# Kernel optimization log

Hardware: AMD Instinct MI355X
Metric: run time of the kernel (lower is better)

## Reference

```python
import jax, jax.numpy as jnp
import numpy as np

K = 16
NUM_RBF = 32
MAX_DIST = 24.0
OUT_DIM = 256
_SPACING = MAX_DIST / (NUM_RBF - 1)
GAMMA = 1.0 / (_SPACING * _SPACING + 1e-08)
CENTERS = jnp.linspace(0.0, MAX_DIST, NUM_RBF)


def setup_inputs() -> dict:
    key = jax.random.key(0)
    k1, k2, k3 = jax.random.split(key, 3)
    B, M = 64, 1024
    # scale coords so pairwise distances span roughly [0, MAX_DIST]
    ligand_coords = jax.random.normal(k1, (B, M, 3), dtype=jnp.float32) * 8.0
    ligand_mask = jax.random.randint(k2, (B, M), 0, 2) > 0
    proj_w = jax.random.normal(k3, (OUT_DIM, K * NUM_RBF), dtype=jnp.float32) * 0.05
    return {"ligand_coords": ligand_coords, "ligand_mask": ligand_mask, "proj_w": proj_w}


def reference(ligand_coords, ligand_mask, proj_w):
    B, M, _ = ligand_coords.shape
    x = ligand_coords.astype(jnp.float32)
    # pairwise euclidean distances via the gram trick (avoids [B,M,M,3])
    sq = jnp.sum(x * x, axis=-1)                      # [B, M]
    gram = jnp.einsum('bid,bjd->bij', x, x)           # [B, M, M]
    d2 = sq[:, :, None] + sq[:, None, :] - 2.0 * gram
    dists = jnp.sqrt(jnp.maximum(d2, 1e-12))          # [B, M, M]
    eye = jnp.eye(M, dtype=bool)[None]
    valid_pair = ligand_mask[:, :, None] & ligand_mask[:, None, :]
    invalid = eye | ~valid_pair
    dists = jnp.where(invalid, jnp.inf, dists)
    # k smallest distances per atom
    neg_topk, _ = jax.lax.top_k(-dists, K)            # [B, M, K]
    topk = -neg_topk
    d_padded = jnp.where(jnp.isfinite(topk), topk, MAX_DIST)
    # RBF embed
    diff = d_padded[..., None] - CENTERS              # [B, M, K, NUM_RBF]
    rbf = jnp.exp(-GAMMA * diff * diff)
    rbf_flat = rbf.reshape(B, M, K * NUM_RBF)
    out = jnp.einsum('bmf,of->bmo', rbf_flat, proj_w)
    return out * ligand_mask[..., None].astype(out.dtype)
```

## Files before the change

kernel.cpp:

```cpp
#include <hip/hip_runtime.h>
#include <hip/hip_bf16.h>
#include <math.h>

#define MDIM 1024
#define QTOT 65536
#define KTOP 16
#define ODIM 256
#define FDIM 512

typedef float f32x4 __attribute__((ext_vector_type(4)));
typedef short s16x8 __attribute__((ext_vector_type(8)));
typedef unsigned u32x4 __attribute__((ext_vector_type(4)));

#define VMIN(a,b)  ({float r_; asm("v_min_f32 %0,%1,%2":"=v"(r_):"v"(a),"v"(b)); r_;})
#define VMAX(a,b)  ({float r_; asm("v_max_f32 %0,%1,%2":"=v"(r_):"v"(a),"v"(b)); r_;})
#define VEXP2(x)   ({float r_; asm("v_exp_f32 %0,%1":"=v"(r_):"v"(x)); r_;})

__device__ __forceinline__ int read_mask(const void* m, int i, bool is8) {
  return is8 ? (int)((const unsigned char*)m)[i] : ((const int*)m)[i];
}

__device__ __forceinline__ unsigned pack2(float lo, float hi) {
  __hip_bfloat162 h = __float22bfloat162_rn(make_float2(lo, hi));
  unsigned u;
  __builtin_memcpy(&u, &h, sizeof(u));
  return u;
}

#define CEx(A,i,j) { float mn_ = VMIN(A[i], A[j]); float mx_ = VMAX(A[i], A[j]); A[i] = mn_; A[j] = mx_; }
#define SORT8(A) \
  CEx(A,0,1) CEx(A,2,3) CEx(A,4,5) CEx(A,6,7) \
  CEx(A,0,2) CEx(A,1,3) CEx(A,4,6) CEx(A,5,7) \
  CEx(A,1,2) CEx(A,5,6) \
  CEx(A,0,4) CEx(A,1,5) CEx(A,2,6) CEx(A,3,7) \
  CEx(A,2,4) CEx(A,3,5) \
  CEx(A,1,2) CEx(A,3,4) CEx(A,5,6)
#define CLEAN16(A) \
  CEx(A,0,8) CEx(A,1,9) CEx(A,2,10) CEx(A,3,11) CEx(A,4,12) CEx(A,5,13) CEx(A,6,14) CEx(A,7,15) \
  CEx(A,0,4) CEx(A,1,5) CEx(A,2,6)  CEx(A,3,7)  CEx(A,8,12) CEx(A,9,13) CEx(A,10,14) CEx(A,11,15) \
  CEx(A,0,2) CEx(A,1,3) CEx(A,4,6)  CEx(A,5,7)  CEx(A,8,10) CEx(A,9,11) CEx(A,12,14) CEx(A,13,15) \
  CEx(A,0,1) CEx(A,2,3) CEx(A,4,5)  CEx(A,6,7)  CEx(A,8,9)  CEx(A,10,11) CEx(A,12,13) CEx(A,14,15)

__global__ __launch_bounds__(256) void wconv_kernel(
    const float* __restrict__ W, u32x4* __restrict__ Wb)
{
  int slot = blockIdx.x * 256 + threadIdx.x;
  int cg = slot >> 10;
  int rem = slot & 1023;
  int s = rem >> 6, l = rem & 63;
  int col = cg * 16 + (l & 15);
  int kk = s * 32 + (l >> 4) * 8;
  const float4* p = (const float4*)(W + (size_t)col * FDIM + kk);
  float4 a = p[0], b = p[1];
  u32x4 u0;
  u0[0] = pack2(a.x, a.y); u0[1] = pack2(a.z, a.w);
  u0[2] = pack2(b.x, b.y); u0[3] = pack2(b.z, b.w);
  Wb[(size_t)(cg * 16 + s) * 64 + l] = u0;
}

constexpr double SPd = 24.0 / 31.0;
constexpr double SP2d = SPd * SPd;
constexpr float ALPHA = (float)(-(SP2d / (SP2d + 1e-8)) * 1.4426950408889634);
constexpr float INV_SP = (float)(1.0 / SPd);

__device__ __forceinline__ void gen_cell(u32x4* Ab, int rf, int rowlo, int s, float d0) {
  float d = (d0 < 0.f) ? 1.0e9f : d0;
  float u = d * INV_SP;
  float C1 = (-2.0f * ALPHA) * u;
  float C0 = ALPHA * u * u;
  #pragma unroll
  for (int c8 = 0; c8 < 4; ++c8) {
    u32x4 ch;
    #pragma unroll
    for (int q = 0; q < 4; ++q) {
      const int j0 = c8 * 8 + q * 2;
      float e0 = VEXP2(fmaf(C1, (float)j0,       C0) + ALPHA * (float)(j0 * j0));
      float e1 = VEXP2(fmaf(C1, (float)(j0 + 1), C0) + ALPHA * (float)((j0 + 1) * (j0 + 1)));
      ch[q] = pack2(e0, e1);
    }
    Ab[rf * 1040 + s * 65 + c8 * 16 + rowlo] = ch;
  }
}

__global__ __launch_bounds__(512, 6) void fused_kernel(
    const float* __restrict__ coords, const void* __restrict__ mask,
    const u32x4* __restrict__ Wb, float* __restrict__ out)
{
  __shared__ __align__(16) char raw[66560];
  __shared__ float dvals[64][17];
  __shared__ int s_cnt;
  __shared__ int s_is8;

  float4* pts = (float4*)raw;
  short* posof = (short*)(raw + 16384);
  float* ST = (float*)(raw + 18432);
  u32x4* Ab = (u32x4*)raw;

  const int tid = threadIdx.x;
  const int lane = tid & 63;
  const int wv = tid >> 6;
  const int bid = blockIdx.x;
  const int batch = bid >> 4;
  const int qchunk = bid & 15;

  if (tid == 0) { s_cnt = 0; s_is8 = 0; }
  __syncthreads();
  {
    unsigned w = ((const unsigned*)mask)[tid & 255];
    if (w > 1u) atomicOr(&s_is8, 1);
  }
  __syncthreads();
  const bool is8 = (s_is8 != 0);

  const float* cb = coords + (size_t)batch * MDIM * 3;
  const int mbase = batch * MDIM;

  #pragma unroll
  for (int r = 0; r < 2; ++r) {
    int a = r * 512 + tid;
    int v = read_mask(mask, mbase + a, is8);
    float x = cb[a*3+0], y = cb[a*3+1], z = cb[a*3+2];
    float S = fmaf(z, z, fmaf(y, y, x * x));
    unsigned long long bal = __ballot(v != 0);
    int base = 0;
    if (lane == 0) base = atomicAdd(&s_cnt, __popcll(bal));
    base = __shfl(base, 0);
    int pos = base + __popcll(bal & ((1ull << lane) - 1ull));
    if (v) {
      float4 p; p.x = x; p.y = y; p.z = z; p.w = S;
      pts[pos] = p;
    }
    posof[a] = (short)(v ? pos : -1);
  }
  __syncthreads();
  const int cnt = s_cnt;
  const int cntP = (cnt + 63) & ~63;
  for (int i = cnt + tid; i < cntP; i += 512) {
    float4 p; p.x = 0.f; p.y = 0.f; p.z = 0.f; p.w = 3.0e38f;
    pts[i] = p;
  }
  __syncthreads();

  const int qlocal = qchunk * 64 + lane;
  const float qx = cb[qlocal*3+0], qy = cb[qlocal*3+1], qz = cb[qlocal*3+2];
  const float Q = fmaf(qz, qz, fmaf(qy, qy, qx * qx));
  const float m2x = -2.0f * qx, m2y = -2.0f * qy, m2z = -2.0f * qz;
  const int selfpos = posof[qlocal];
  const int G = cntP >> 3;
  const int sbase = wv * G;

  float t[16];
  #pragma unroll
  for (int i = 0; i < 16; ++i) t[i] = 3.0e38f;

  for (int b = 0; b < G; b += 8) {
    float s[8];
    #pragma unroll
    for (int i = 0; i < 8; ++i) {
      const int idx = sbase + b + i;
      float4 p = pts[idx];
      float d = fmaf(p.z, m2z, fmaf(p.y, m2y, fmaf(p.x, m2x, p.w)));
      s[i] = (idx == selfpos) ? 3.0e38f : d;
    }
    SORT8(s)
    #pragma unroll
    for (int i = 0; i < 8; ++i) t[8 + i] = VMIN(t[8 + i], s[7 - i]);
    CLEAN16(t)
  }

  {
    float* dst = ST + (wv * 64 + lane) * 17;
    #pragma unroll
    for (int i = 0; i < 16; ++i) dst[i] = t[i];
  }
  __syncthreads();

  if (wv == 0) {
    float m0[16];
    const float* l0 = ST + lane * 17;
    #pragma unroll
    for (int i = 0; i < 16; ++i) m0[i] = l0[i];
    for (int sl = 1; sl < 8; ++sl) {
      const float* ls = ST + (sl * 64 + lane) * 17;
      float o[16], m[16];
      #pragma unroll
      for (int i = 0; i < 16; ++i) o[i] = ls[i];
      #pragma unroll
      for (int i = 0; i < 16; ++i) m[i] = VMIN(m0[i], o[15 - i]);
      CLEAN16(m)
      #pragma unroll
      for (int i = 0; i < 16; ++i) m0[i] = m[i];
    }
    int mq = read_mask(mask, mbase + qlocal, is8);
    #pragma unroll
    for (int i = 0; i < 16; ++i) {
      float v = m0[i];
      float d = (v > 1.0e37f) ? 24.0f : sqrtf(fmaxf(v + Q, 1e-12f));
      dvals[lane][i] = mq ? d : -1.0f;
    }
  }
  __syncthreads();

  #pragma unroll
  for (int i = 0; i < 2; ++i) {
    int cellid = tid + 512 * i;
    int row = cellid >> 4, slot = cellid & 15;
    gen_cell(Ab, row >> 4, row & 15, slot, dvals[row][slot]);
  }
  __syncthreads();

  f32x4 acc[4][2];
  #pragma unroll
  for (int rf = 0; rf < 4; ++rf)
    #pragma unroll
    for (int e = 0; e < 2; ++e) acc[rf][e] = (f32x4){0.f, 0.f, 0.f, 0.f};

  u32x4 bcur[2], bnxt[2];
  #pragma unroll
  for (int e = 0; e < 2; ++e)
    bcur[e] = Wb[(size_t)((e * 8 + wv) * 16) * 64 + lane];

  #pragma unroll
  for (int s = 0; s < 16; ++s) {
    if (s < 15) {
      #pragma unroll
      for (int e = 0; e < 2; ++e)
        bnxt[e] = Wb[(size_t)((e * 8 + wv) * 16 + s + 1) * 64 + lane];
    }
    s16x8 a[4], b[2];
    #pragma unroll
    for (int rf = 0; rf < 4; ++rf) {
      u32x4 ra = Ab[rf * 1040 + s * 65 + lane];
      __builtin_memcpy(&a[rf], &ra, sizeof(ra));
    }
    #pragma unroll
    for (int e = 0; e < 2; ++e) __builtin_memcpy(&b[e], &bcur[e], sizeof(u32x4));
    #pragma unroll
    for (int rf = 0; rf < 4; ++rf)
      #pragma unroll
      for (int e = 0; e < 2; ++e)
        acc[rf][e] = __builtin_amdgcn_mfma_f32_16x16x32_bf16(a[rf], b[e], acc[rf][e], 0, 0, 0);
    #pragma unroll
    for (int e = 0; e < 2; ++e) bcur[e] = bnxt[e];
  }

  const int qbase = mbase + qchunk * 64;
  const int rb_ = (lane >> 4) * 4;
  #pragma unroll
  for (int rf = 0; rf < 4; ++rf) {
    #pragma unroll
    for (int e = 0; e < 2; ++e) {
      const int col = (e * 8 + wv) * 16 + (lane & 15);
      #pragma unroll
      for (int r = 0; r < 4; ++r)
        out[(size_t)(qbase + rf * 16 + rb_ + r) * ODIM + col] = acc[rf][e][r];
    }
  }
}

extern "C" void kernel_launch(void* const* d_in, const int* in_sizes, int n_in,
                              void* d_out, int out_size, void* d_ws, size_t ws_size,
                              hipStream_t stream) {
  const float* coords = (const float*)d_in[0];
  const void* mask = d_in[1];
  const float* W = (const float*)d_in[2];
  float* out = (float*)d_out;
  u32x4* Wb = (u32x4*)d_ws;

  hipLaunchKernelGGL(wconv_kernel, dim3(64), dim3(256), 0, stream, W, Wb);
  hipLaunchKernelGGL(fused_kernel, dim3(QTOT / 64), dim3(512), 0, stream,
                     coords, mask, Wb, out);
}
```

Baseline: 54.04 us.

## Keep top-8 per slice with exact fallback to full top-16 merge

Each wave now tracks only the 8 smallest squared distances per query in its slice, using a cheaper 8-wide merge network instead of the 16-wide one, and drops the per-element self-index check. The final merge removes the self entry from the slice that holds it and combines the eight top-8 lists into a top-16. If any slice's 8th value is below the merged 16th, meaning that slice might have had more qualifying candidates, a block-wide flag triggers a full recompute with the original top-16 path. This trades a much cheaper main loop for an extra merge and a possible full rescan when the fallback fires.

```diff
diff --git a/kernel.cpp b/kernel.cpp
--- a/kernel.cpp
+++ b/kernel.cpp
@@ -35,6 +35,10 @@
   CEx(A,0,4) CEx(A,1,5) CEx(A,2,6) CEx(A,3,7) \
   CEx(A,2,4) CEx(A,3,5) \
   CEx(A,1,2) CEx(A,3,4) CEx(A,5,6)
+#define CLEAN8(A) \
+  CEx(A,0,4) CEx(A,1,5) CEx(A,2,6) CEx(A,3,7) \
+  CEx(A,0,2) CEx(A,1,3) CEx(A,4,6) CEx(A,5,7) \
+  CEx(A,0,1) CEx(A,2,3) CEx(A,4,5) CEx(A,6,7)
 #define CLEAN16(A) \
   CEx(A,0,8) CEx(A,1,9) CEx(A,2,10) CEx(A,3,11) CEx(A,4,12) CEx(A,5,13) CEx(A,6,14) CEx(A,7,15) \
   CEx(A,0,4) CEx(A,1,5) CEx(A,2,6)  CEx(A,3,7)  CEx(A,8,12) CEx(A,9,13) CEx(A,10,14) CEx(A,11,15) \
@@ -90,6 +94,7 @@
   __shared__ float dvals[64][17];
   __shared__ int s_cnt;
   __shared__ int s_is8;
+  __shared__ int s_fb;
 
   float4* pts = (float4*)raw;
   short* posof = (short*)(raw + 16384);
@@ -103,7 +108,7 @@
   const int batch = bid >> 4;
   const int qchunk = bid & 15;
 
-  if (tid == 0) { s_cnt = 0; s_is8 = 0; }
+  if (tid == 0) { s_cnt = 0; s_is8 = 0; s_fb = 0; }
   __syncthreads();
   {
     unsigned w = ((const unsigned*)mask)[tid & 255];
@@ -149,57 +154,126 @@
   const int G = cntP >> 3;
   const int sbase = wv * G;
 
-  float t[16];
-  #pragma unroll
-  for (int i = 0; i < 16; ++i) t[i] = 3.0e38f;
+  float t8[8];
+  #pragma unroll
+  for (int i = 0; i < 8; ++i) t8[i] = 3.0e38f;
 
   for (int b = 0; b < G; b += 8) {
     float s[8];
     #pragma unroll
     for (int i = 0; i < 8; ++i) {
-      const int idx = sbase + b + i;
-      float4 p = pts[idx];
-      float d = fmaf(p.z, m2z, fmaf(p.y, m2y, fmaf(p.x, m2x, p.w)));
-      s[i] = (idx == selfpos) ? 3.0e38f : d;
+      float4 p = pts[sbase + b + i];
+      s[i] = fmaf(p.z, m2z, fmaf(p.y, m2y, fmaf(p.x, m2x, p.w)));
     }
     SORT8(s)
-    #pragma unroll
-    for (int i = 0; i < 8; ++i) t[8 + i] = VMIN(t[8 + i], s[7 - i]);
-    CLEAN16(t)
+    float m[8];
+    #pragma unroll
+    for (int i = 0; i < 8; ++i) m[i] = VMIN(t8[i], s[7 - i]);
+    CLEAN8(m)
+    #pragma unroll
+    for (int i = 0; i < 8; ++i) t8[i] = m[i];
   }
 
   {
-    float* dst = ST + (wv * 64 + lane) * 17;
-    #pragma unroll
-    for (int i = 0; i < 16; ++i) dst[i] = t[i];
+    float* dst = ST + (wv * 64 + lane) * 9;
+    #pragma unroll
+    for (int i = 0; i < 8; ++i) dst[i] = t8[i];
   }
   __syncthreads();
 
   if (wv == 0) {
-    float m0[16];
-    const float* l0 = ST + lane * 17;
-    #pragma unroll
-    for (int i = 0; i < 16; ++i) m0[i] = l0[i];
+    int selfslice = 0;
+    if (selfpos >= 0) {
+      #pragma unroll
+      for (int sl = 1; sl < 8; ++sl) selfslice += (selfpos >= sl * G) ? 1 : 0;
+    } else {
+      selfslice = -1;
+    }
+    float t16[16];
+    float bmin;
+    {
+      const float* ls = ST + lane * 9;
+      int sh = (selfslice == 0) ? 1 : 0;
+      #pragma unroll
+      for (int i = 0; i < 7; ++i) t16[i] = ls[i + sh];
+      t16[7] = sh ? 3.0e38f : ls[7];
+      #pragma unroll
+      for (int i = 8; i < 16; ++i) t16[i] = 3.0e38f;
+      bmin = ls[7];
+    }
     for (int sl = 1; sl < 8; ++sl) {
-      const float* ls = ST + (sl * 64 + lane) * 17;
-      float o[16], m[16];
-      #pragma unroll
-      for (int i = 0; i < 16; ++i) o[i] = ls[i];
-      #pragma unroll
-      for (int i = 0; i < 16; ++i) m[i] = VMIN(m0[i], o[15 - i]);
-      CLEAN16(m)
-      #pragma unroll
-      for (int i = 0; i < 16; ++i) m0[i] = m[i];
-    }
+      const float* ls = ST + (sl * 64 + lane) * 9;
+      int sh = (selfslice == sl) ? 1 : 0;
+      float o[8];
+      #pragma unroll
+      for (int i = 0; i < 7; ++i) o[i] = ls[i + sh];
+      o[7] = sh ? 3.0e38f : ls[7];
+      bmin = VMIN(bmin, ls[7]);
+      #pragma unroll
+      for (int i = 0; i < 8; ++i) t16[8 + i] = VMIN(t16[8 + i], o[7 - i]);
+      CLEAN16(t16)
+    }
+    if (bmin < t16[15]) atomicOr(&s_fb, 1);
     int mq = read_mask(mask, mbase + qlocal, is8);
     #pragma unroll
     for (int i = 0; i < 16; ++i) {
-      float v = m0[i];
+      float v = t16[i];
       float d = (v > 1.0e37f) ? 24.0f : sqrtf(fmaxf(v + Q, 1e-12f));
       dvals[lane][i] = mq ? d : -1.0f;
     }
   }
   __syncthreads();
+
+  if (s_fb != 0) {
+    float t[16];
+    #pragma unroll
+    for (int i = 0; i < 16; ++i) t[i] = 3.0e38f;
+    for (int b = 0; b < G; b += 8) {
+      float s[8];
+      #pragma unroll
+      for (int i = 0; i < 8; ++i) {
+        const int idx = sbase + b + i;
+        float4 p = pts[idx];
+        float d = fmaf(p.z, m2z, fmaf(p.y, m2y, fmaf(p.x, m2x, p.w)));
+        s[i] = (idx == selfpos) ? 3.0e38f : d;
+      }
+      SORT8(s)
+      #pragma unroll
+      for (int i = 0; i < 8; ++i) t[8 + i] = VMIN(t[8 + i], s[7 - i]);
+      CLEAN16(t)
+    }
+    {
+      float* dst = ST + (wv * 64 + lane) * 17;
+      #pragma unroll
+      for (int i = 0; i < 16; ++i) dst[i] = t[i];
+    }
+    __syncthreads();
+    if (wv == 0) {
+      float m0[16];
+      const float* l0 = ST + lane * 17;
+      #pragma unroll
+      for (int i = 0; i < 16; ++i) m0[i] = l0[i];
+      for (int sl = 1; sl < 8; ++sl) {
+        const float* ls = ST + (sl * 64 + lane) * 17;
+        float o[16], m[16];
+        #pragma unroll
+        for (int i = 0; i < 16; ++i) o[i] = ls[i];
+        #pragma unroll
+        for (int i = 0; i < 16; ++i) m[i] = VMIN(m0[i], o[15 - i]);
+        CLEAN16(m)
+        #pragma unroll
+        for (int i = 0; i < 16; ++i) m0[i] = m[i];
+      }
+      int mq = read_mask(mask, mbase + qlocal, is8);
+      #pragma unroll
+      for (int i = 0; i < 16; ++i) {
+        float v = m0[i];
+        float d = (v > 1.0e37f) ? 24.0f : sqrtf(fmaxf(v + Q, 1e-12f));
+        dvals[lane][i] = mq ? d : -1.0f;
+      }
+    }
+    __syncthreads();
+  }
 
   #pragma unroll
   for (int i = 0; i < 2; ++i) {
```

Result: slower. 60.82 us (+12.5%).
